# Kernel optimization log

Hardware: AMD Instinct MI355X
Metric: run time of the kernel (lower is better)

The kernel has to match this reference:

```python
import jax, jax.numpy as jnp
import numpy as np

DIM = 2048      # model dim
H = 32          # num_heads
N = 128         # state_dim
G = 1           # num_groups
K = 4           # conv_size
HID = 4096     # hidden_dim = multiple_of*ceil(2.0*DIM/256)
P = HID // H    # head_dim = 128
CHUNK = 256
EPS = 1e-6
DT_MIN, DT_MAX = 0.001, 0.1


def setup_inputs() -> dict:
    key = jax.random.key(0)
    ks = jax.random.split(key, 8)
    b, s = 2, 2048
    d_in = 2 * HID + 2 * G * N + H           # 8448
    conv_dim = HID + 2 * G * N               # 4352
    return {
        "x": jax.random.normal(ks[0], (b, s, DIM), jnp.float32),
        "W_in": jax.random.normal(ks[1], (d_in, DIM), jnp.float32) / np.sqrt(DIM),
        "conv_w": jax.random.normal(ks[2], (conv_dim, K), jnp.float32) / np.sqrt(K),
        "conv_b": jnp.zeros((conv_dim,), jnp.float32),
        "dt_bias": jnp.zeros((H,), jnp.float32),
        "A_log": jnp.log(jax.random.uniform(ks[3], (H,), jnp.float32, 1.0, 16.0)),
        "D": jnp.ones((H,), jnp.float32),
        "norm_w": jnp.ones((HID,), jnp.float32),
        "W_out": jax.random.normal(ks[4], (DIM, HID), jnp.float32) / np.sqrt(HID),
    }


def _causal_conv_silu(xBC, w, bias):
    # depthwise causal conv1d, kernel K, then SiLU. xBC: (b,s,c), w: (c,K)
    b, s, c = xBC.shape
    xp = jnp.pad(xBC, ((0, 0), (K - 1, 0), (0, 0)))
    y = sum(xp[:, k:k + s, :] * w[:, k] for k in range(K)) + bias
    return jax.nn.silu(y)


def _chunked_scan(x, dt, A, B, C, D):
    # Mamba2 chunked selective scan.
    # x:(b,s,h,p) dt:(b,s,h) A:(h,) B,C:(b,s,n) (groups=1) D:(h,)
    b, s, h, p = x.shape
    n = B.shape[-1]
    nc, L = s // CHUNK, CHUNK
    xc = x.reshape(b, nc, L, h, p)
    dtc = dt.reshape(b, nc, L, h)
    Bc = B.reshape(b, nc, L, n)
    Cc = C.reshape(b, nc, L, n)

    dA = dtc * A                          # (b,nc,L,h), A<0
    dA_cs = jnp.cumsum(dA, axis=2)        # (b,nc,L,h)

    # intra-chunk contribution
    seg = dA_cs[:, :, :, None, :] - dA_cs[:, :, None, :, :]   # (b,nc,L,L,h)
    mask = jnp.tril(jnp.ones((L, L), bool))[None, None, :, :, None]
    decay = jnp.exp(jnp.where(mask, seg, -jnp.inf))
    CB = jnp.einsum('bcln,bcsn->bcls', Cc, Bc)                # (b,nc,L,L)
    y_intra = jnp.einsum('bcls,bclsh,bcsh,bcshp->bclhp', CB, decay, dtc, xc)

    # per-chunk final states
    decay_states = jnp.exp(dA_cs[:, :, -1:, :] - dA_cs)       # (b,nc,L,h)
    states = jnp.einsum('bclh,bclh,bclhp,bcln->bchpn', decay_states, dtc, xc, Bc)

    # inter-chunk recurrence over chunk index
    dA_chunk = dA_cs[:, :, -1, :]                              # (b,nc,h)
    def step(prev, inp):
        st, dec = inp
        new = prev * jnp.exp(dec)[:, :, None, None] + st
        return new, prev
    init = jnp.zeros((b, h, p, n), x.dtype)
    _, prev_states = jax.lax.scan(step, init,
                                  (jnp.moveaxis(states, 1, 0), jnp.moveaxis(dA_chunk, 1, 0)))
    prev_states = jnp.moveaxis(prev_states, 0, 1)              # state at start of each chunk

    y_inter = jnp.einsum('bcln,bclh,bchpn->bclhp', Cc, jnp.exp(dA_cs), prev_states)
    y = (y_intra + y_inter).reshape(b, s, h, p)
    return y + x * D[None, None, :, None]


def reference(x, W_in, conv_w, conv_b, dt_bias, A_log, D, norm_w, W_out):
    b, s, _ = x.shape
    zxbcdt = x @ W_in.T                                        # (b,s,2*HID+2GN+H)
    z, xBC, dt = jnp.split(zxbcdt, [HID, 2 * HID + 2 * G * N], axis=-1)
    xBC = _causal_conv_silu(xBC, conv_w, conv_b)
    xs, B, C = jnp.split(xBC, [HID, HID + G * N], axis=-1)
    A = -jnp.exp(A_log)
    dt = jnp.clip(jax.nn.softplus(dt + dt_bias), DT_MIN, DT_MAX)
    xs = xs.reshape(b, s, H, P)
    y = _chunked_scan(xs, dt, A, B, C, D).reshape(b, s, HID)
    y = y * jax.nn.silu(z)                                     # gate, norm_before_gate=False
    y = y * jax.lax.rsqrt(jnp.mean(y * y, axis=-1, keepdims=True) + EPS) * norm_w
    return y @ W_out.T
```

## Files before the change

kernel.cpp:

```cpp
#include <hip/hip_runtime.h>


typedef short s16x8 __attribute__((ext_vector_type(8)));
typedef float f32x4 __attribute__((ext_vector_type(4)));

__device__ __forceinline__ float bf2f(ushort u) {
    return __builtin_bit_cast(float, (unsigned)u << 16);
}
__device__ __forceinline__ ushort f2bf(float f) {
    unsigned u = __builtin_bit_cast(unsigned, f);
    unsigned r = u + 0x7fffu + ((u >> 16) & 1u);
    return (ushort)(r >> 16);
}

__device__ __forceinline__ void gld16(const void* g, void* l) {
    __builtin_amdgcn_global_load_lds((__attribute__((address_space(1))) void*)g,
                                     (__attribute__((address_space(3))) void*)l, 16, 0, 0);
}

#define BARRIER() asm volatile("s_barrier" ::: "memory")

__global__ void cast_all_k(const float4* __restrict__ x, const float4* __restrict__ wout,
                           const float4* __restrict__ win, ushort* __restrict__ xb,
                           ushort* __restrict__ woutb, ushort* __restrict__ winb) {
    const long b = blockIdx.x, tid = threadIdx.x;
    if (b < 8192) {
        long i = b * 256 + tid;
        float4 v = x[i];
        ushort4 o = { f2bf(v.x), f2bf(v.y), f2bf(v.z), f2bf(v.w) };
        *(ushort4*)(xb + i * 4) = o;
    } else if (b < 16384) {
        long i = (b - 8192) * 256 + tid;
        float4 v = wout[i];
        ushort4 o = { f2bf(v.x), f2bf(v.y), f2bf(v.z), f2bf(v.w) };
        *(ushort4*)(woutb + i * 4) = o;
    } else {
        long i = (b - 16384) * 256 + tid;
        ushort4 o;
        if (i < 4341760L) {
            float4 v = win[i];
            o = { f2bf(v.x), f2bf(v.y), f2bf(v.z), f2bf(v.w) };
        } else {
            o = { 0, 0, 0, 0 };
        }
        *(ushort4*)(winb + i * 4) = o;
    }
}

__global__ __launch_bounds__(512, 1) void gemm1_k(const ushort* __restrict__ A,
                                                  const ushort* __restrict__ Bm,
                                                  ushort* __restrict__ zbuf,
                                                  ushort* __restrict__ xbc,
                                                  ushort* __restrict__ dtr) {
    constexpr int K = 2048, NT = 64;
    __shared__ ushort lds[3 * 8192 + 3 * 6144];
    const int tid = threadIdx.x, lane = tid & 63, wave = tid >> 6;
    const int wm = wave >> 2, wn = wave & 3;
    const int bid = blockIdx.x;
    const int xcd = bid & 7, w = bid >> 3;
    const int mt = xcd * 2 + (w & 1), nt = w >> 1;
    const long m0 = (long)mt * 256, n0 = (long)nt * 192;

    const int st_row = lane >> 2;
    const int st_gc = ((lane & 3) * 8) ^ (((lane >> 5) & 1) << 4);

    auto STAGE_A = [&](int buf, int kt) {
#pragma unroll
        for (int j = 0; j < 2; j++) {
            int sidx = wave + j * 8;
            gld16(A + (m0 + sidx * 16 + st_row) * K + kt + st_gc,
                  lds + buf * 8192 + sidx * 512 + lane * 8);
        }
    };
    auto STAGE_B = [&](int buf, int kt) {
#pragma unroll
        for (int j = 0; j < 2; j++) {
            int sidx = wave + j * 8;
            if (sidx < 12)
                gld16(Bm + (n0 + sidx * 16 + st_row) * K + kt + st_gc,
                      lds + 24576 + buf * 6144 + sidx * 512 + lane * 8);
        }
    };

    const int cfr = (lane >> 4) * 8;
    const int lr = lane & 15;
    auto LDFA = [&](int buf, int r) -> s16x8 {
        int off = buf * 8192 + ((r >> 4) << 9) + ((r & 15) << 5)
                + (cfr ^ (((r >> 3) & 1) << 4));
        return *(const s16x8*)(lds + off);
    };
    auto LDFB = [&](int buf, int r) -> s16x8 {
        int off = 24576 + buf * 6144 + ((r >> 4) << 9) + ((r & 15) << 5)
                + (cfr ^ (((r >> 3) & 1) << 4));
        return *(const s16x8*)(lds + off);
    };

    f32x4 zero = { 0.f, 0.f, 0.f, 0.f };
    f32x4 acc[8][3];
#pragma unroll
    for (int i = 0; i < 8; i++)
#pragma unroll
        for (int j = 0; j < 3; j++) acc[i][j] = zero;

    STAGE_A(0, 0);  STAGE_B(0, 0);
    STAGE_A(1, 32); STAGE_B(1, 32);
    asm volatile("s_waitcnt vmcnt(3)" ::: "memory");
    BARRIER();

    for (int t = 0; t < NT; ++t) {
        const int cur = t % 3;
        const int nxt = (t + 2) % 3;
        const int kt2 = (t + 2) * 32;
        const bool do_stage = (t + 2) < NT;

        s16x8 bfr[3], alo[4], ahi[4];
#pragma unroll
        for (int ni = 0; ni < 3; ni++) bfr[ni] = LDFB(cur, wn * 48 + ni * 16 + lr);
#pragma unroll
        for (int mi = 0; mi < 4; mi++) alo[mi] = LDFA(cur, wm * 128 + mi * 16 + lr);
#pragma unroll
        for (int mi = 0; mi < 4; mi++) ahi[mi] = LDFA(cur, wm * 128 + 64 + mi * 16 + lr);
        if (do_stage) { STAGE_A(nxt, kt2); STAGE_B(nxt, kt2); }

        __builtin_amdgcn_s_setprio(1);
#pragma unroll
        for (int mi = 0; mi < 4; mi++)
#pragma unroll
            for (int ni = 0; ni < 3; ni++)
                acc[mi][ni] = __builtin_amdgcn_mfma_f32_16x16x32_bf16(alo[mi], bfr[ni], acc[mi][ni], 0, 0, 0);
#pragma unroll
        for (int mi = 0; mi < 4; mi++)
#pragma unroll
            for (int ni = 0; ni < 3; ni++)
                acc[mi + 4][ni] = __builtin_amdgcn_mfma_f32_16x16x32_bf16(ahi[mi], bfr[ni], acc[mi + 4][ni], 0, 0, 0);
        __builtin_amdgcn_s_setprio(0);

        if (do_stage) asm volatile("s_waitcnt vmcnt(3)" ::: "memory");
        else          asm volatile("s_waitcnt vmcnt(0)" ::: "memory");
        BARRIER();
    }

    const int lr4 = (lane >> 4) * 4;
#pragma unroll
    for (int mi = 0; mi < 8; mi++) {
#pragma unroll
        for (int ni = 0; ni < 3; ni++) {
            const long col = n0 + wn * 48 + ni * 16 + lr;
            ushort* dst;
            long stride;
            if (col < 4096)      { dst = zbuf + col;         stride = 4096; }
            else if (col < 8448) { dst = xbc + (col - 4096); stride = 4352; }
            else if (col < 8480) { dst = dtr + (col - 8448); stride = 32;   }
            else continue;
            const long row0 = m0 + wm * 128 + mi * 16 + lr4;
#pragma unroll
            for (int r = 0; r < 4; r++) dst[(row0 + r) * stride] = f2bf(acc[mi][ni][r]);
        }
    }
}

__global__ __launch_bounds__(256) void gemm2_k(const ushort* __restrict__ A,
                                               const ushort* __restrict__ Bm,
                                               float* __restrict__ Cout) {
    constexpr int K = 4096, NT = 128;
    __shared__ ushort lds[2 * 4096 + 2 * 4096];
    const int tid = threadIdx.x, lane = tid & 63, wave = tid >> 6;
    const int wm = wave >> 1, wn = wave & 1;
    const int bid = blockIdx.x;
    const int xcd = bid & 7, w = bid >> 3;
    const int mt = xcd * 4 + (w & 3), nt = w >> 2;
    const long m0 = (long)mt * 128, n0 = (long)nt * 128;

    const int st_row = lane >> 2;
    const int st_gc = ((lane & 3) * 8) ^ (((lane >> 5) & 1) << 4);

    auto STAGE = [&](int buf, int kt) {
#pragma unroll
        for (int j = 0; j < 2; j++) {
            int sidx = wave + j * 4;
            gld16(A + (m0 + sidx * 16 + st_row) * K + kt + st_gc,
                  lds + buf * 4096 + sidx * 512 + lane * 8);
        }
#pragma unroll
        for (int j = 0; j < 2; j++) {
            int sidx = wave + j * 4;
            gld16(Bm + (n0 + sidx * 16 + st_row) * K + kt + st_gc,
                  lds + 8192 + buf * 4096 + sidx * 512 + lane * 8);
        }
    };

    const int cfr = (lane >> 4) * 8;
    const int lr = lane & 15;
    auto LDFA = [&](int buf, int r) -> s16x8 {
        int off = buf * 4096 + ((r >> 4) << 9) + ((r & 15) << 5)
                + (cfr ^ (((r >> 3) & 1) << 4));
        return *(const s16x8*)(lds + off);
    };
    auto LDFB = [&](int buf, int r) -> s16x8 {
        int off = 8192 + buf * 4096 + ((r >> 4) << 9) + ((r & 15) << 5)
                + (cfr ^ (((r >> 3) & 1) << 4));
        return *(const s16x8*)(lds + off);
    };

    f32x4 zero = { 0.f, 0.f, 0.f, 0.f };
    f32x4 acc[4][4];
#pragma unroll
    for (int i = 0; i < 4; i++)
#pragma unroll
        for (int j = 0; j < 4; j++) acc[i][j] = zero;

    STAGE(0, 0);
    asm volatile("s_waitcnt vmcnt(0)" ::: "memory");
    BARRIER();

    for (int t = 0; t < NT; ++t) {
        const int cur = t & 1;
        if ((t + 1) < NT) STAGE((t + 1) & 1, (t + 1) * 32);

        s16x8 af[4], bf[4];
#pragma unroll
        for (int mi = 0; mi < 4; mi++) af[mi] = LDFA(cur, wm * 64 + mi * 16 + lr);
#pragma unroll
        for (int ni = 0; ni < 4; ni++) bf[ni] = LDFB(cur, wn * 64 + ni * 16 + lr);

        __builtin_amdgcn_s_setprio(1);
#pragma unroll
        for (int mi = 0; mi < 4; mi++)
#pragma unroll
            for (int ni = 0; ni < 4; ni++)
                acc[mi][ni] = __builtin_amdgcn_mfma_f32_16x16x32_bf16(af[mi], bf[ni], acc[mi][ni], 0, 0, 0);
        __builtin_amdgcn_s_setprio(0);

        asm volatile("s_waitcnt vmcnt(0)" ::: "memory");
        BARRIER();
    }

    const long crow = m0 + wm * 64 + ((lane >> 4) << 2);
    const long ccol = n0 + wn * 64 + (lane & 15);
#pragma unroll
    for (int mi = 0; mi < 4; mi++)
#pragma unroll
        for (int ni = 0; ni < 4; ni++)
#pragma unroll
            for (int r = 0; r < 4; r++)
                Cout[(crow + mi * 16 + r) * 2048 + ccol + ni * 16] = acc[mi][ni][r];
}

__global__ __launch_bounds__(256) void convx_k(const ushort* __restrict__ xbc,
                                               const float* __restrict__ w,
                                               const float* __restrict__ bias,
                                               ushort* __restrict__ xbcc,
                                               ushort* __restrict__ xT,
                                               ushort* __restrict__ Bt) {
    __shared__ ushort xin[35][136];
    __shared__ ushort yL[32][132];
    const int stile = blockIdx.x, slot = blockIdx.y, bc = blockIdx.z;
    const int tid = threadIdx.x;
    const int cc = bc & 7;
    const long tbase = (long)bc * 256 + stile * 32;
    const int c0 = slot * 128;
    const bool head = (cc == 0 && stile == 0);

#pragma unroll
    for (int i = 0; i < 3; i++) {
        int u = tid + i * 256;
        if (u < 560) {
            int r = u >> 4, seg = u & 15;
            s16x8 v;
            if (head && r < 3) {
#pragma unroll
                for (int j = 0; j < 8; j++) v[j] = 0;
            } else {
                v = *(const s16x8*)&xbc[(tbase - 3 + r) * 4352 + c0 + seg * 8];
            }
            *(s16x8*)&xin[r][seg * 8] = v;
        }
    }
    __syncthreads();

    const int s_loc = tid >> 3, p0 = (tid & 7) * 16;
    ushort yo[16];
#pragma unroll
    for (int j = 0; j < 16; j++) {
        int c = p0 + j;
        float a = bias[c0 + c];
#pragma unroll
        for (int k = 0; k < 4; k++)
            a += bf2f(xin[s_loc + k][c]) * w[(c0 + c) * 4 + k];
        float yv = a / (1.f + __expf(-a));
        ushort ub = f2bf(yv);
        yo[j] = ub;
        yL[s_loc][c] = ub;
    }
    *(s16x8*)&xbcc[(tbase + s_loc) * 4352 + c0 + p0] = *(const s16x8*)&yo[0];
    *(s16x8*)&xbcc[(tbase + s_loc) * 4352 + c0 + p0 + 8] = *(const s16x8*)&yo[8];
    __syncthreads();

    if (slot < 33) {
        const int p = tid >> 1, s0 = (tid & 1) * 16;
        ushort o[16];
#pragma unroll
        for (int j = 0; j < 16; j++) o[j] = yL[s0 + j][p];
        ushort* dst = (slot < 32)
            ? (xT + ((long)(bc * 32 + slot) * 128 + p) * 256 + stile * 32 + s0)
            : (Bt + ((long)bc * 128 + p) * 256 + stile * 32 + s0);
        *(s16x8*)&dst[0] = *(const s16x8*)&o[0];
        *(s16x8*)&dst[8] = *(const s16x8*)&o[8];
    }
}

__global__ void prep_k(const ushort* __restrict__ dtr, const float* __restrict__ dt_bias,
                       const float* __restrict__ A_log, float* __restrict__ dtp,
                       float* __restrict__ dacs) {
    const int bx = blockIdx.x;
    const int h = bx & 31, cc = (bx >> 5) & 7, bi = bx >> 8;
    const int lane = threadIdx.x;
    const float A = -__expf(A_log[h]);
    const float bsh = dt_bias[h];
    float v[4], cs[4];
    float run = 0.f;
#pragma unroll
    for (int j = 0; j < 4; j++) {
        int pos = cc * 256 + lane * 4 + j;
        float raw = bf2f(dtr[((long)(bi * 2048 + pos)) * 32 + h]) + bsh;
        float sp = (raw > 20.f) ? raw : log1pf(__expf(raw));
        float d = fminf(fmaxf(sp, 0.001f), 0.1f);
        v[j] = d;
        run += d * A;
        cs[j] = run;
    }
    float tot = run, pre = run;
    for (int off = 1; off < 64; off <<= 1) {
        float u = __shfl_up(pre, off, 64);
        if (lane >= off) pre += u;
    }
    float excl = pre - tot;
    const long base = ((long)(bi * 32 + h)) * 2048 + cc * 256 + lane * 4;
#pragma unroll
    for (int j = 0; j < 4; j++) { dtp[base + j] = v[j]; dacs[base + j] = excl + cs[j]; }
}

__global__ __launch_bounds__(256) void cb_mfma_k(const ushort* __restrict__ xbcc,
                                                 float* __restrict__ CB) {
    const int bid = blockIdx.x;
    const int sq = bid & 1, lq = (bid >> 1) & 1, bc = bid >> 2;
    const int tid = threadIdx.x, lane = tid & 63, wave = tid >> 6;
    const int wm = wave >> 1, wn = wave & 1;
    const long tbase = (long)bc * 256;

    f32x4 zero = { 0.f, 0.f, 0.f, 0.f };
    f32x4 acc[4][4];
#pragma unroll
    for (int i = 0; i < 4; i++)
#pragma unroll
        for (int j = 0; j < 4; j++) acc[i][j] = zero;

    for (int kst = 0; kst < 4; ++kst) {
        const int koff = kst * 32 + (lane >> 4) * 8;
        s16x8 a[4], b[4];
#pragma unroll
        for (int mi = 0; mi < 4; mi++) {
            int l = lq * 128 + wm * 64 + mi * 16 + (lane & 15);
            a[mi] = *(const s16x8*)&xbcc[(tbase + l) * 4352 + 4224 + koff];
        }
#pragma unroll
        for (int ni = 0; ni < 4; ni++) {
            int s = sq * 128 + wn * 64 + ni * 16 + (lane & 15);
            b[ni] = *(const s16x8*)&xbcc[(tbase + s) * 4352 + 4096 + koff];
        }
#pragma unroll
        for (int mi = 0; mi < 4; mi++)
#pragma unroll
            for (int ni = 0; ni < 4; ni++)
                acc[mi][ni] = __builtin_amdgcn_mfma_f32_16x16x32_bf16(a[mi], b[ni], acc[mi][ni], 0, 0, 0);
    }

    float* out = CB + (long)bc * 65536;
#pragma unroll
    for (int mi = 0; mi < 4; mi++)
#pragma unroll
        for (int ni = 0; ni < 4; ni++)
#pragma unroll
            for (int r = 0; r < 4; r++) {
                int l = lq * 128 + wm * 64 + mi * 16 + (lane >> 4) * 4 + r;
                int s = sq * 128 + wn * 64 + ni * 16 + (lane & 15);
                out[(long)l * 256 + s] = acc[mi][ni][r];
            }
}

__global__ __launch_bounds__(256) void scan_mfma_k(const ushort* __restrict__ xT,
                                                   const float* __restrict__ CB,
                                                   const float* __restrict__ dtp,
                                                   const float* __restrict__ dacs,
                                                   const ushort* __restrict__ xbcc,
                                                   const float* __restrict__ st,
                                                   ushort* __restrict__ yh) {
    const int bx = blockIdx.x;
    const int ltile = bx & 1, h = (bx >> 1) & 31, cc = (bx >> 6) & 7, bi = bx >> 9;
    const int tid = threadIdx.x, lane = tid & 63, wave = tid >> 6;
    const int wm = wave >> 1, wn = wave & 1;

    __shared__ float dA_s[256];
    __shared__ float F_s[256];

    const long dbase = ((long)(bi * 32 + h)) * 2048 + cc * 256;
    {
        float a = dacs[dbase + tid];
        float r = dacs[dbase + (tid | 31)];
        dA_s[tid] = a;
        F_s[tid] = __expf(r - a) * dtp[dbase + tid];
    }
    __syncthreads();

    int lch[4];
    float dAl[4];
#pragma unroll
    for (int mi = 0; mi < 4; mi++) {
        lch[mi] = ltile * 128 + wm * 64 + mi * 16 + (lane & 15);
        dAl[mi] = dA_s[lch[mi]];
    }

    f32x4 zero = { 0.f, 0.f, 0.f, 0.f };
    f32x4 acc[4][4];
#pragma unroll
    for (int i = 0; i < 4; i++)
#pragma unroll
        for (int j = 0; j < 4; j++) acc[i][j] = zero;

    const long tbase = (long)bi * 2048 + cc * 256;
    const long cbbase = ((long)(bi * 8 + cc)) * 65536;
    const ushort* xrow = xT + (((long)(bi * 8 + cc) * 32 + h) * 128) * 256;
    const int nsb = ltile * 4 + 4;

    for (int sb = 0; sb < nsb; ++sb) {
        const int soff = sb * 32 + (lane >> 4) * 8;
        s16x8 bf[4];
#pragma unroll
        for (int ni = 0; ni < 4; ni++) {
            int p = wn * 64 + ni * 16 + (lane & 15);
            bf[ni] = *(const s16x8*)&xrow[(long)p * 256 + soff];
        }
        const float Rsb = dA_s[sb * 32 + 31];
        const int s0 = soff;
#pragma unroll
        for (int mi = 0; mi < 4; mi++) {
            const int lb = lch[mi] >> 5;
            if (sb > lb) continue;
            const float* cbrow = CB + cbbase + (long)lch[mi] * 256 + s0;
            float4 c0 = *(const float4*)cbrow;
            float4 c1 = *(const float4*)(cbrow + 4);
            float E = __expf(dAl[mi] - Rsb);
            float m[8];
            m[0] = c0.x * E * F_s[s0 + 0]; m[1] = c0.y * E * F_s[s0 + 1];
            m[2] = c0.z * E * F_s[s0 + 2]; m[3] = c0.w * E * F_s[s0 + 3];
            m[4] = c1.x * E * F_s[s0 + 4]; m[5] = c1.y * E * F_s[s0 + 5];
            m[6] = c1.z * E * F_s[s0 + 6]; m[7] = c1.w * E * F_s[s0 + 7];
            if (sb == lb) {
#pragma unroll
                for (int j = 0; j < 8; j++)
                    if (s0 + j > lch[mi]) m[j] = 0.f;
            }
            s16x8 a;
#pragma unroll
            for (int j = 0; j < 8; j++) a[j] = (short)f2bf(m[j]);
#pragma unroll
            for (int ni = 0; ni < 4; ni++)
                acc[mi][ni] = __builtin_amdgcn_mfma_f32_16x16x32_bf16(a, bf[ni], acc[mi][ni], 0, 0, 0);
        }
    }

    const float* sbase = st + (((long)(bi * 8 + cc) * 32 + h) * 128) * 128;
    float eAr[4];
#pragma unroll
    for (int mi = 0; mi < 4; mi++) eAr[mi] = __expf(dAl[mi]);
    for (int kk = 0; kk < 4; ++kk) {
        const int koff = kk * 32 + (lane >> 4) * 8;
        s16x8 a[4], b[4];
#pragma unroll
        for (int mi = 0; mi < 4; mi++) {
            s16x8 raw = *(const s16x8*)&xbcc[(tbase + lch[mi]) * 4352 + 4224 + koff];
#pragma unroll
            for (int j = 0; j < 8; j++)
                a[mi][j] = (short)f2bf(bf2f((ushort)raw[j]) * eAr[mi]);
        }
#pragma unroll
        for (int ni = 0; ni < 4; ni++) {
            int p = wn * 64 + ni * 16 + (lane & 15);
            const float* pr = sbase + (long)p * 128 + koff;
            float4 v0 = *(const float4*)pr;
            float4 v1 = *(const float4*)(pr + 4);
            b[ni][0] = (short)f2bf(v0.x); b[ni][1] = (short)f2bf(v0.y);
            b[ni][2] = (short)f2bf(v0.z); b[ni][3] = (short)f2bf(v0.w);
            b[ni][4] = (short)f2bf(v1.x); b[ni][5] = (short)f2bf(v1.y);
            b[ni][6] = (short)f2bf(v1.z); b[ni][7] = (short)f2bf(v1.w);
        }
#pragma unroll
        for (int mi = 0; mi < 4; mi++)
#pragma unroll
            for (int ni = 0; ni < 4; ni++)
                acc[mi][ni] = __builtin_amdgcn_mfma_f32_16x16x32_bf16(a[mi], b[ni], acc[mi][ni], 0, 0, 0);
    }

    const long crow = tbase + ltile * 128 + wm * 64 + ((lane >> 4) << 2);
    const int ccol = h * 128 + wn * 64 + (lane & 15);
#pragma unroll
    for (int mi = 0; mi < 4; mi++)
#pragma unroll
        for (int ni = 0; ni < 4; ni++)
#pragma unroll
            for (int r = 0; r < 4; r++)
                yh[(crow + mi * 16 + r) * 4096 + ccol + ni * 16] = f2bf(acc[mi][ni][r]);
}

__global__ __launch_bounds__(256) void states_mfma_k(const ushort* __restrict__ xT,
                                                     const ushort* __restrict__ Bt,
                                                     const float* __restrict__ dtp,
                                                     const float* __restrict__ dacs,
                                                     float* __restrict__ states) {
    const int bx = blockIdx.x;
    const int h = bx & 31, cc = (bx >> 5) & 7, bi = bx >> 8;
    const int bc = bi * 8 + cc;
    const int tid = threadIdx.x, lane = tid & 63, wave = tid >> 6;
    const int wm = wave >> 1, wn = wave & 1;
    __shared__ float wl[256];
    const long dbase = ((long)(bi * 32 + h)) * 2048 + cc * 256;
    {
        float last = dacs[dbase + 255];
        wl[tid] = __expf(last - dacs[dbase + tid]) * dtp[dbase + tid];
    }
    __syncthreads();

    f32x4 zero = { 0.f, 0.f, 0.f, 0.f };
    f32x4 acc[4][4];
#pragma unroll
    for (int i = 0; i < 4; i++)
#pragma unroll
        for (int j = 0; j < 4; j++) acc[i][j] = zero;

    const ushort* xrow = xT + (((long)bc * 32 + h) * 128) * 256;
    const ushort* brow = Bt + ((long)bc * 128) * 256;

    for (int sb = 0; sb < 8; ++sb) {
        const int soff = sb * 32 + (lane >> 4) * 8;
        s16x8 a[4], b[4];
#pragma unroll
        for (int mi = 0; mi < 4; mi++) {
            int p = wm * 64 + mi * 16 + (lane & 15);
            s16x8 raw = *(const s16x8*)&xrow[(long)p * 256 + soff];
#pragma unroll
            for (int j = 0; j < 8; j++)
                a[mi][j] = (short)f2bf(bf2f((ushort)raw[j]) * wl[soff + j]);
        }
#pragma unroll
        for (int ni = 0; ni < 4; ni++) {
            int n = wn * 64 + ni * 16 + (lane & 15);
            b[ni] = *(const s16x8*)&brow[(long)n * 256 + soff];
        }
#pragma unroll
        for (int mi = 0; mi < 4; mi++)
#pragma unroll
            for (int ni = 0; ni < 4; ni++)
                acc[mi][ni] = __builtin_amdgcn_mfma_f32_16x16x32_bf16(a[mi], b[ni], acc[mi][ni], 0, 0, 0);
    }

    float* out = states + (((long)bc * 32 + h) * 128) * 128;
#pragma unroll
    for (int mi = 0; mi < 4; mi++)
#pragma unroll
        for (int ni = 0; ni < 4; ni++)
#pragma unroll
            for (int r = 0; r < 4; r++) {
                int p = wm * 64 + mi * 16 + (lane >> 4) * 4 + r;
                int n = wn * 64 + ni * 16 + (lane & 15);
                out[(long)p * 128 + n] = acc[mi][ni][r];
            }
}

__global__ void rec_k(float* __restrict__ states, const float* __restrict__ dacs) {
    const int i = blockIdx.x * 256 + threadIdx.x;
    const int n = i & 127, p = (i >> 7) & 127, h = (i >> 14) & 31, bi = i >> 19;
    const long dbase = ((long)(bi * 32 + h)) * 2048;
    float run = 0.f;
    for (int cc = 0; cc < 8; cc++) {
        const long off = ((((long)(bi * 8 + cc)) * 32 + h) * 128 + p) * 128 + n;
        float st = states[off];
        states[off] = run;
        float dec = dacs[dbase + cc * 256 + 255];
        run = run * __expf(dec) + st;
    }
}

__global__ __launch_bounds__(256) void gate_rms_k(const ushort* __restrict__ yh, const ushort* __restrict__ zbuf,
                                                  const ushort* __restrict__ xbcc, const float* __restrict__ Dv,
                                                  const float* __restrict__ norm_w, ushort* __restrict__ yb) {
    const int t = blockIdx.x, tid = threadIdx.x;
    const ushort* yr = &yh[(long)t * 4096];
    const ushort* zr = &zbuf[(long)t * 4096];
    const ushort* xr = &xbcc[(long)t * 4352];
    float g[16];
    float ss = 0.f;
#pragma unroll
    for (int j = 0; j < 16; j++) {
        int i = j * 256 + tid;
        float z = bf2f(zr[i]);
        float yv = bf2f(yr[i]) + Dv[i >> 7] * bf2f(xr[i]);
        float gv = yv * (z / (1.f + __expf(-z)));
        g[j] = gv;
        ss += gv * gv;
    }
#pragma unroll
    for (int off = 32; off > 0; off >>= 1) ss += __shfl_xor(ss, off, 64);
    __shared__ float red[4];
    if ((tid & 63) == 0) red[tid >> 6] = ss;
    __syncthreads();
    float tot = red[0] + red[1] + red[2] + red[3];
    float sc = rsqrtf(tot * (1.f / 4096.f) + 1e-6f);
#pragma unroll
    for (int j = 0; j < 16; j++) {
        int i = j * 256 + tid;
        yb[(long)t * 4096 + i] = f2bf(g[j] * sc * norm_w[i]);
    }
}

extern "C" void kernel_launch(void* const* d_in, const int* in_sizes, int n_in,
                              void* d_out, int out_size, void* d_ws, size_t ws_size,
                              hipStream_t stream) {
    const float* x       = (const float*)d_in[0];
    const float* W_in    = (const float*)d_in[1];
    const float* conv_w  = (const float*)d_in[2];
    const float* conv_b  = (const float*)d_in[3];
    const float* dt_bias = (const float*)d_in[4];
    const float* A_log   = (const float*)d_in[5];
    const float* Dv      = (const float*)d_in[6];
    const float* norm_w  = (const float*)d_in[7];
    const float* W_out   = (const float*)d_in[8];

    char* w8 = (char*)d_ws;
    ushort* xb    = (ushort*)(w8 + 0L);
    ushort* xT    = (ushort*)(w8 + 0L);
    ushort* yb    = (ushort*)(w8 + 0L);
    ushort* woutb = (ushort*)(w8 + 33554432L);
    ushort* Bt    = (ushort*)(w8 + 50331648L);
    ushort* zbuf  = (ushort*)(w8 + 52428800L);
    ushort* xbc   = (ushort*)(w8 + 85983232L);
    ushort* dtr   = (ushort*)(w8 + 121634816L);
    ushort* xbcc  = (ushort*)(w8 + 121896960L);
    float*  dtp   = (float*)(w8 + 157548544L);
    float*  dacs  = (float*)(w8 + 158072832L);
    float*  cb    = (float*)(w8 + 158597120L);
    ushort* yh    = (ushort*)(w8 + 162791424L);
    ushort* winb  = (ushort*)(w8 + 162791424L);
    float*  st    = (float*)(w8 + 229900288L);

    cast_all_k<<<34048, 256, 0, stream>>>((const float4*)x, (const float4*)W_out,
                                          (const float4*)W_in, xb, woutb, winb);
    gemm1_k<<<736, 512, 0, stream>>>(xb, winb, zbuf, xbc, dtr);
    convx_k<<<dim3(8, 34, 16), 256, 0, stream>>>(xbc, conv_w, conv_b, xbcc, xT, Bt);
    prep_k<<<512, 64, 0, stream>>>(dtr, dt_bias, A_log, dtp, dacs);
    cb_mfma_k<<<64, 256, 0, stream>>>(xbcc, cb);
    states_mfma_k<<<512, 256, 0, stream>>>(xT, Bt, dtp, dacs, st);
    rec_k<<<4096, 256, 0, stream>>>(st, dacs);
    scan_mfma_k<<<1024, 256, 0, stream>>>(xT, cb, dtp, dacs, xbcc, st, yh);
    gate_rms_k<<<4096, 256, 0, stream>>>(yh, zbuf, xbcc, Dv, norm_w, yb);
    gemm2_k<<<512, 256, 0, stream>>>(yb, woutb, (float*)d_out);
}
```

Measured before the change: 459.3 us.

## Restructure gemm1 mainloop into double-buffered BK=64 with four interleaved compute phases

The input projection GEMM moves from a triple-buffered BK=32 pipeline to a double-buffered BK=64 pipeline, halving the number of main-loop iterations. Each iteration is split into four phases that interleave LDS fragment reads, staging of the next tile's global loads, and MFMA blocks, with barriers between phases. This is in the spirit of ping-pong scheduling, meant to overlap memory with compute and cut per-iteration loop overhead. The cost is more barriers per iteration and a full vmcnt(0) wait at the end of each iteration, which may expose global load latency.

```diff
diff --git a/kernel.cpp b/kernel.cpp
--- a/kernel.cpp
+++ b/kernel.cpp
@@ -52,8 +52,8 @@
                                                   ushort* __restrict__ zbuf,
                                                   ushort* __restrict__ xbc,
                                                   ushort* __restrict__ dtr) {
-    constexpr int K = 2048, NT = 64;
-    __shared__ ushort lds[3 * 8192 + 3 * 6144];
+    constexpr int K = 2048, NT = 32;
+    __shared__ ushort lds[2 * 28672];
     const int tid = threadIdx.x, lane = tid & 63, wave = tid >> 6;
     const int wm = wave >> 2, wn = wave & 3;
     const int bid = blockIdx.x;
@@ -64,33 +64,33 @@
     const int st_row = lane >> 2;
     const int st_gc = ((lane & 3) * 8) ^ (((lane >> 5) & 1) << 4);
 
-    auto STAGE_A = [&](int buf, int kt) {
+    auto STAGE_A = [&](int buf, int kt, int kb) {
 #pragma unroll
         for (int j = 0; j < 2; j++) {
             int sidx = wave + j * 8;
-            gld16(A + (m0 + sidx * 16 + st_row) * K + kt + st_gc,
-                  lds + buf * 8192 + sidx * 512 + lane * 8);
+            gld16(A + (m0 + sidx * 16 + st_row) * K + kt + kb * 32 + st_gc,
+                  lds + buf * 28672 + kb * 8192 + sidx * 512 + lane * 8);
         }
     };
-    auto STAGE_B = [&](int buf, int kt) {
+    auto STAGE_B = [&](int buf, int kt, int kb) {
 #pragma unroll
         for (int j = 0; j < 2; j++) {
             int sidx = wave + j * 8;
             if (sidx < 12)
-                gld16(Bm + (n0 + sidx * 16 + st_row) * K + kt + st_gc,
-                      lds + 24576 + buf * 6144 + sidx * 512 + lane * 8);
+                gld16(Bm + (n0 + sidx * 16 + st_row) * K + kt + kb * 32 + st_gc,
+                      lds + buf * 28672 + 16384 + kb * 6144 + sidx * 512 + lane * 8);
         }
     };
 
     const int cfr = (lane >> 4) * 8;
     const int lr = lane & 15;
-    auto LDFA = [&](int buf, int r) -> s16x8 {
-        int off = buf * 8192 + ((r >> 4) << 9) + ((r & 15) << 5)
+    auto LDFA = [&](int buf, int r, int kb) -> s16x8 {
+        int off = buf * 28672 + kb * 8192 + ((r >> 4) << 9) + ((r & 15) << 5)
                 + (cfr ^ (((r >> 3) & 1) << 4));
         return *(const s16x8*)(lds + off);
     };
-    auto LDFB = [&](int buf, int r) -> s16x8 {
-        int off = 24576 + buf * 6144 + ((r >> 4) << 9) + ((r & 15) << 5)
+    auto LDFB = [&](int buf, int r, int kb) -> s16x8 {
+        int off = buf * 28672 + 16384 + kb * 6144 + ((r >> 4) << 9) + ((r & 15) << 5)
                 + (cfr ^ (((r >> 3) & 1) << 4));
         return *(const s16x8*)(lds + off);
     };
@@ -102,41 +102,93 @@
 #pragma unroll
         for (int j = 0; j < 3; j++) acc[i][j] = zero;
 
-    STAGE_A(0, 0);  STAGE_B(0, 0);
-    STAGE_A(1, 32); STAGE_B(1, 32);
-    asm volatile("s_waitcnt vmcnt(3)" ::: "memory");
+    STAGE_A(0, 0, 0); STAGE_A(0, 0, 1);
+    STAGE_B(0, 0, 0); STAGE_B(0, 0, 1);
+    asm volatile("s_waitcnt vmcnt(0)" ::: "memory");
     BARRIER();
 
     for (int t = 0; t < NT; ++t) {
-        const int cur = t % 3;
-        const int nxt = (t + 2) % 3;
-        const int kt2 = (t + 2) * 32;
-        const bool do_stage = (t + 2) < NT;
-
-        s16x8 bfr[3], alo[4], ahi[4];
-#pragma unroll
-        for (int ni = 0; ni < 3; ni++) bfr[ni] = LDFB(cur, wn * 48 + ni * 16 + lr);
-#pragma unroll
-        for (int mi = 0; mi < 4; mi++) alo[mi] = LDFA(cur, wm * 128 + mi * 16 + lr);
-#pragma unroll
-        for (int mi = 0; mi < 4; mi++) ahi[mi] = LDFA(cur, wm * 128 + 64 + mi * 16 + lr);
-        if (do_stage) { STAGE_A(nxt, kt2); STAGE_B(nxt, kt2); }
-
+        const int cur = t & 1, nxt = cur ^ 1;
+        const int ktn = (t + 1) * 64;
+        const bool ds = (t + 1) < NT;
+
+        s16x8 bfr[3][2];
+        s16x8 aq[2][2];
+
+#pragma unroll
+        for (int ni = 0; ni < 3; ni++)
+#pragma unroll
+            for (int kk = 0; kk < 2; kk++)
+                bfr[ni][kk] = LDFB(cur, wn * 48 + ni * 16 + lr, kk);
+#pragma unroll
+        for (int m2 = 0; m2 < 2; m2++)
+#pragma unroll
+            for (int kk = 0; kk < 2; kk++)
+                aq[m2][kk] = LDFA(cur, wm * 128 + m2 * 16 + lr, kk);
+        if (ds) { STAGE_A(nxt, ktn, 0); STAGE_B(nxt, ktn, 0); }
+        BARRIER();
         __builtin_amdgcn_s_setprio(1);
 #pragma unroll
-        for (int mi = 0; mi < 4; mi++)
+        for (int m2 = 0; m2 < 2; m2++)
 #pragma unroll
             for (int ni = 0; ni < 3; ni++)
-                acc[mi][ni] = __builtin_amdgcn_mfma_f32_16x16x32_bf16(alo[mi], bfr[ni], acc[mi][ni], 0, 0, 0);
-#pragma unroll
-        for (int mi = 0; mi < 4; mi++)
+#pragma unroll
+                for (int kk = 0; kk < 2; kk++)
+                    acc[m2][ni] = __builtin_amdgcn_mfma_f32_16x16x32_bf16(aq[m2][kk], bfr[ni][kk], acc[m2][ni], 0, 0, 0);
+        __builtin_amdgcn_s_setprio(0);
+        BARRIER();
+
+#pragma unroll
+        for (int m2 = 0; m2 < 2; m2++)
+#pragma unroll
+            for (int kk = 0; kk < 2; kk++)
+                aq[m2][kk] = LDFA(cur, wm * 128 + (2 + m2) * 16 + lr, kk);
+        if (ds) { STAGE_A(nxt, ktn, 1); STAGE_B(nxt, ktn, 1); }
+        BARRIER();
+        __builtin_amdgcn_s_setprio(1);
+#pragma unroll
+        for (int m2 = 0; m2 < 2; m2++)
 #pragma unroll
             for (int ni = 0; ni < 3; ni++)
-                acc[mi + 4][ni] = __builtin_amdgcn_mfma_f32_16x16x32_bf16(ahi[mi], bfr[ni], acc[mi + 4][ni], 0, 0, 0);
+#pragma unroll
+                for (int kk = 0; kk < 2; kk++)
+                    acc[2 + m2][ni] = __builtin_amdgcn_mfma_f32_16x16x32_bf16(aq[m2][kk], bfr[ni][kk], acc[2 + m2][ni], 0, 0, 0);
         __builtin_amdgcn_s_setprio(0);
-
-        if (do_stage) asm volatile("s_waitcnt vmcnt(3)" ::: "memory");
-        else          asm volatile("s_waitcnt vmcnt(0)" ::: "memory");
+        BARRIER();
+
+#pragma unroll
+        for (int m2 = 0; m2 < 2; m2++)
+#pragma unroll
+            for (int kk = 0; kk < 2; kk++)
+                aq[m2][kk] = LDFA(cur, wm * 128 + (4 + m2) * 16 + lr, kk);
+        BARRIER();
+        __builtin_amdgcn_s_setprio(1);
+#pragma unroll
+        for (int m2 = 0; m2 < 2; m2++)
+#pragma unroll
+            for (int ni = 0; ni < 3; ni++)
+#pragma unroll
+                for (int kk = 0; kk < 2; kk++)
+                    acc[4 + m2][ni] = __builtin_amdgcn_mfma_f32_16x16x32_bf16(aq[m2][kk], bfr[ni][kk], acc[4 + m2][ni], 0, 0, 0);
+        __builtin_amdgcn_s_setprio(0);
+        BARRIER();
+
+#pragma unroll
+        for (int m2 = 0; m2 < 2; m2++)
+#pragma unroll
+            for (int kk = 0; kk < 2; kk++)
+                aq[m2][kk] = LDFA(cur, wm * 128 + (6 + m2) * 16 + lr, kk);
+        BARRIER();
+        __builtin_amdgcn_s_setprio(1);
+#pragma unroll
+        for (int m2 = 0; m2 < 2; m2++)
+#pragma unroll
+            for (int ni = 0; ni < 3; ni++)
+#pragma unroll
+                for (int kk = 0; kk < 2; kk++)
+                    acc[6 + m2][ni] = __builtin_amdgcn_mfma_f32_16x16x32_bf16(aq[m2][kk], bfr[ni][kk], acc[6 + m2][ni], 0, 0, 0);
+        __builtin_amdgcn_s_setprio(0);
+        asm volatile("s_waitcnt vmcnt(0)" ::: "memory");
         BARRIER();
     }
 
```

New measurement: 459.2 us. Within noise of the previous version (-0.0%).
